# Kernel tuning notes

Hardware: AMD Instinct MI355X
Metric: run time of the kernel (lower is better)

The kernel has to match this reference:

```python
import jax, jax.numpy as jnp
import numpy as np

EPS = 0.97  # ContrastLoss eps
T = 0.07    # temperature

def _embed(x, W, b):
    # Linear + L2 normalize (Normalize(power=2))
    h = x @ W.T + b                     # [B, feat_dim]
    norm = jnp.sqrt(jnp.sum(h * h, axis=1, keepdims=True))
    return h / norm

def setup_inputs() -> dict:
    key = jax.random.key(0)
    ks = jax.random.split(key, 7)
    B, S, Td, F = 8192, 2048, 2048, 128
    return {
        "f_s": jax.random.normal(ks[0], (B, S), jnp.float32),
        "f_t": jax.random.normal(ks[1], (B, Td), jnp.float32),
        "y": jax.random.randint(ks[2], (B,), 0, 100, jnp.int64),
        "W_s": jax.random.normal(ks[3], (F, S), jnp.float32) * 0.02,
        "b_s": jax.random.normal(ks[4], (F,), jnp.float32) * 0.02,
        "W_t": jax.random.normal(ks[5], (F, Td), jnp.float32) * 0.02,
        "b_t": jax.random.normal(ks[6], (F,), jnp.float32) * 0.02,
    }

def reference(f_s, f_t, y, W_s, b_s, W_t, b_t):
    fs = _embed(f_s, W_s, b_s)
    ft = _embed(f_t, W_t, b_t)
    # CRDLoss re-normalizes (idempotent, kept for fidelity)
    fs = fs / jnp.linalg.norm(fs, axis=1, keepdims=True)
    ft = ft / jnp.linalg.norm(ft, axis=1, keepdims=True)
    bsz = fs.shape[0]
    x = jnp.exp((fs @ ft.T) / T)  # [B, B] exponentiated similarities
    same = y[None, :] == y[:, None]        # y_expand == y_expand.T
    diag = jnp.eye(bsz, dtype=bool)
    pos_mask = same & ~diag
    neg_mask = ~same & ~diag
    # masked log-ratio sums instead of dynamic-shape gathers
    log_D1 = jnp.log(x / (x + EPS))
    log_D0 = jnp.log(EPS / (x + EPS))
    loss = -(jnp.sum(jnp.where(pos_mask, log_D1, 0.0))
             + jnp.sum(jnp.where(neg_mask, log_D0, 0.0))) / bsz
    return loss
```

## Files before the change

kernel.cpp:

```cpp
#include <hip/hip_runtime.h>
#include <math.h>


typedef _Float16 half_t;
typedef half_t halfx4 __attribute__((ext_vector_type(4)));
typedef half_t halfx8 __attribute__((ext_vector_type(8)));
typedef float f32x4 __attribute__((ext_vector_type(4)));

#define B_TOT   8192
#define K_EMB   2048
#define F_DIM   128
#define INV_T   14.285714285714286f
#define EPS_C   0.97f
#define LOG_EPS (-0.030459207485f)

__global__ __launch_bounds__(256) void cvt_w_kernel(
    const float* __restrict__ Ws, const float* __restrict__ Wt,
    half_t* __restrict__ Ws16, half_t* __restrict__ Wt16)
{
    const float* src = blockIdx.y ? Wt : Ws;
    half_t* dst = blockIdx.y ? Wt16 : Ws16;
    int pos4 = blockIdx.x * 256 + threadIdx.x;
    float4 v = *(const float4*)(src + (size_t)pos4 * 4);
    halfx4 h4 = {(half_t)v.x, (half_t)v.y, (half_t)v.z, (half_t)v.w};
    *(halfx4*)(dst + (size_t)pos4 * 4) = h4;
}

__global__ __launch_bounds__(256) void embed_kernel(
    const float* __restrict__ Xs, const float* __restrict__ Xt,
    const half_t* __restrict__ Ws16, const half_t* __restrict__ Wt16,
    const float* __restrict__ bs, const float* __restrict__ bt,
    half_t* __restrict__ outs, half_t* __restrict__ outt)
{
    const float* X; const half_t* W16; const float* bias; half_t* out;
    if (blockIdx.y == 0) { X = Xs; W16 = Ws16; bias = bs; out = outs; }
    else                 { X = Xt; W16 = Wt16; bias = bt; out = outt; }

    __shared__ half_t As[2][32][72];
    __shared__ half_t Bs[2][128][72];
    __shared__ float  biasS[128];
    __shared__ float  redS[32][2];
    __shared__ float  invS[32];

    const int tid = threadIdx.x;
    const int r0  = blockIdx.x * 32;
    if (tid < 128) biasS[tid] = bias[tid];

    const int lane = tid & 63;
    const int w    = tid >> 6;
    const int wm   = w & 1, wn = w >> 1;
    const int l16  = lane & 15, lhi = lane >> 4;

    f32x4 acc[4];
    for (int in = 0; in < 4; ++in) acc[in] = f32x4{0.f, 0.f, 0.f, 0.f};

    const int ar0 = tid >> 4, ar1 = (tid + 256) >> 4;
    const int akq = (tid & 15) * 4;
    const int bc  = (tid & 7) * 8;

    float4 na[2]; uint4 nb[4];

    na[0] = *(const float4*)(X + (size_t)(r0 + ar0) * K_EMB + akq);
    na[1] = *(const float4*)(X + (size_t)(r0 + ar1) * K_EMB + akq);
#pragma unroll
    for (int i = 0; i < 4; ++i)
        nb[i] = *(const uint4*)(W16 + (size_t)((tid + i * 256) >> 3) * K_EMB + bc);
    {
        halfx4 h0 = {(half_t)na[0].x, (half_t)na[0].y, (half_t)na[0].z, (half_t)na[0].w};
        halfx4 h1 = {(half_t)na[1].x, (half_t)na[1].y, (half_t)na[1].z, (half_t)na[1].w};
        *(halfx4*)&As[0][ar0][akq] = h0;
        *(halfx4*)&As[0][ar1][akq] = h1;
#pragma unroll
        for (int i = 0; i < 4; ++i)
            *(uint4*)&Bs[0][(tid + i * 256) >> 3][bc] = nb[i];
    }
    __syncthreads();

    for (int it = 0; it < 32; ++it) {
        const int cur = it & 1;
        if (it < 31) {
            const int kb = (it + 1) * 64;
            na[0] = *(const float4*)(X + (size_t)(r0 + ar0) * K_EMB + kb + akq);
            na[1] = *(const float4*)(X + (size_t)(r0 + ar1) * K_EMB + kb + akq);
#pragma unroll
            for (int i = 0; i < 4; ++i)
                nb[i] = *(const uint4*)(W16 + (size_t)((tid + i * 256) >> 3) * K_EMB + kb + bc);
        }
#pragma unroll
        for (int kk = 0; kk < 2; ++kk) {
            halfx8 a, b[4];
            a = *(const halfx8*)&As[cur][wm * 16 + l16][kk * 32 + lhi * 8];
#pragma unroll
            for (int in = 0; in < 4; ++in)
                b[in] = *(const halfx8*)&Bs[cur][wn * 64 + in * 16 + l16][kk * 32 + lhi * 8];
#pragma unroll
            for (int in = 0; in < 4; ++in)
                acc[in] = __builtin_amdgcn_mfma_f32_16x16x32_f16(a, b[in], acc[in], 0, 0, 0);
        }
        if (it < 31) {
            const int nxt = cur ^ 1;
            halfx4 h0 = {(half_t)na[0].x, (half_t)na[0].y, (half_t)na[0].z, (half_t)na[0].w};
            halfx4 h1 = {(half_t)na[1].x, (half_t)na[1].y, (half_t)na[1].z, (half_t)na[1].w};
            *(halfx4*)&As[nxt][ar0][akq] = h0;
            *(halfx4*)&As[nxt][ar1][akq] = h1;
#pragma unroll
            for (int i = 0; i < 4; ++i)
                *(uint4*)&Bs[nxt][(tid + i * 256) >> 3][bc] = nb[i];
        }
        __syncthreads();
    }

    float h[4][4];
    float psum[4];
#pragma unroll
    for (int reg = 0; reg < 4; ++reg) {
        float p = 0.f;
#pragma unroll
        for (int in = 0; in < 4; ++in) {
            int col = wn * 64 + in * 16 + l16;
            float v = acc[in][reg] + biasS[col];
            h[in][reg] = v;
            p += v * v;
        }
        p += __shfl_xor(p, 1);
        p += __shfl_xor(p, 2);
        p += __shfl_xor(p, 4);
        p += __shfl_xor(p, 8);
        psum[reg] = p;
    }
    if (l16 == 0)
#pragma unroll
        for (int reg = 0; reg < 4; ++reg)
            redS[wm * 16 + lhi * 4 + reg][wn] = psum[reg];
    __syncthreads();
    if (tid < 32) invS[tid] = rsqrtf(redS[tid][0] + redS[tid][1]);
    __syncthreads();

#pragma unroll
    for (int in = 0; in < 4; ++in)
#pragma unroll
        for (int reg = 0; reg < 4; ++reg) {
            int row = wm * 16 + lhi * 4 + reg;
            int col = wn * 64 + in * 16 + l16;
            out[(size_t)(r0 + row) * F_DIM + col] = (half_t)(h[in][reg] * invS[row]);
        }
}

__global__ __launch_bounds__(256) void loss_kernel(
    const half_t* __restrict__ FS, const half_t* __restrict__ FT,
    const int* __restrict__ y, double* __restrict__ partials)
{
    __shared__ uint4 As4[128 * 8];
    __shared__ uint4 Bs4[128 * 8];
    __shared__ int   yrl[128], ycl[128];
    __shared__ float wsum[4];

    const int tid = threadIdx.x;
    const int i0  = blockIdx.x * 128;
    const int j0  = blockIdx.y * 128;

    if (tid < 128) yrl[tid] = y[i0 + tid];
    else           ycl[tid - 128] = y[j0 + tid - 128];

    const int lane = tid & 63;
    const int w    = tid >> 6;
    const int wm   = w >> 1, wn = w & 1;
    const int l16  = lane & 15, lhi = lane >> 4;

#pragma unroll
    for (int i = 0; i < 4; ++i) {
        int f = tid + i * 256;
        int row = f >> 3, c = f & 7;
        As4[row * 8 + (c ^ (row & 7))] = *(const uint4*)(FS + (size_t)(i0 + row) * F_DIM + c * 8);
    }
#pragma unroll
    for (int i = 0; i < 4; ++i) {
        int f = tid + i * 256;
        int row = f >> 3, c = f & 7;
        Bs4[row * 8 + (c ^ (row & 7))] = *(const uint4*)(FT + (size_t)(j0 + row) * F_DIM + c * 8);
    }
    __syncthreads();

    f32x4 acc[4][4];
    for (int im = 0; im < 4; ++im)
        for (int in = 0; in < 4; ++in)
            acc[im][in] = f32x4{0.f, 0.f, 0.f, 0.f};

    for (int kc = 0; kc < 2; ++kc) {
#pragma unroll
        for (int kk = 0; kk < 2; ++kk) {
            halfx8 a[4], b[4];
#pragma unroll
            for (int im = 0; im < 4; ++im) {
                int r = wm * 64 + im * 16 + l16;
                a[im] = *(const halfx8*)&As4[r * 8 + ((kk * 4 + lhi) ^ (r & 7))];
            }
#pragma unroll
            for (int in = 0; in < 4; ++in) {
                int r = wn * 64 + in * 16 + l16;
                b[in] = *(const halfx8*)&Bs4[r * 8 + ((kk * 4 + lhi) ^ (r & 7))];
            }
#pragma unroll
            for (int im = 0; im < 4; ++im)
#pragma unroll
                for (int in = 0; in < 4; ++in)
                    acc[im][in] = __builtin_amdgcn_mfma_f32_16x16x32_f16(
                        a[im], b[in], acc[im][in], 0, 0, 0);
        }
        if (kc == 0) {
            __syncthreads();
#pragma unroll
            for (int i = 0; i < 4; ++i) {
                int f = tid + i * 256;
                int row = f >> 3, c = f & 7;
                As4[row * 8 + (c ^ (row & 7))] =
                    *(const uint4*)(FS + (size_t)(i0 + row) * F_DIM + 64 + c * 8);
            }
#pragma unroll
            for (int i = 0; i < 4; ++i) {
                int f = tid + i * 256;
                int row = f >> 3, c = f & 7;
                Bs4[row * 8 + (c ^ (row & 7))] =
                    *(const uint4*)(FT + (size_t)(j0 + row) * F_DIM + 64 + c * 8);
            }
            __syncthreads();
        }
    }

    float local = 0.f;
    for (int im = 0; im < 4; ++im) {
        for (int reg = 0; reg < 4; ++reg) {
            int il = wm * 64 + im * 16 + lhi * 4 + reg;
            int yi = yrl[il];
            int gi = i0 + il;
            for (int in = 0; in < 4; ++in) {
                int jl = wn * 64 + in * 16 + l16;
                float s  = acc[im][in][reg];
                float sT = s * INV_T;
                float e  = __expf(sT);
                float l  = __logf(e + EPS_C);
                float term = (yi == ycl[jl]) ? (sT - l) : (LOG_EPS - l);
                if (gi != (j0 + jl)) local += term;
            }
        }
    }
    for (int m = 1; m < 64; m <<= 1) local += __shfl_xor(local, m);
    if (lane == 0) wsum[w] = local;
    __syncthreads();
    if (tid == 0)
        partials[blockIdx.y * gridDim.x + blockIdx.x] =
            ((double)wsum[0] + (double)wsum[1]) + ((double)wsum[2] + (double)wsum[3]);
}

__global__ __launch_bounds__(256) void finalize_kernel(
    const double* __restrict__ partials, float* __restrict__ out)
{
    __shared__ double sh[4];
    double loc = 0.0;
    for (int i = threadIdx.x; i < 4096; i += 256) loc += partials[i];
    for (int m = 1; m < 64; m <<= 1) loc += __shfl_xor(loc, m);
    int lane = threadIdx.x & 63, w = threadIdx.x >> 6;
    if (lane == 0) sh[w] = loc;
    __syncthreads();
    if (threadIdx.x == 0)
        out[0] = (float)(-(sh[0] + sh[1] + sh[2] + sh[3]) / (double)B_TOT);
}

extern "C" void kernel_launch(void* const* d_in, const int* in_sizes, int n_in,
                              void* d_out, int out_size, void* d_ws, size_t ws_size,
                              hipStream_t stream)
{
    const size_t WS_NEEDED = (64 << 10) + (4 << 20) + (1 << 20);
    if (ws_size < WS_NEEDED) return;

    const float* f_s = (const float*)d_in[0];
    const float* f_t = (const float*)d_in[1];
    const int*   y   = (const int*)d_in[2];
    const float* W_s = (const float*)d_in[3];
    const float* b_s = (const float*)d_in[4];
    const float* W_t = (const float*)d_in[5];
    const float* b_t = (const float*)d_in[6];
    float* out = (float*)d_out;

    char* ws = (char*)d_ws;
    double* partials = (double*)ws;
    half_t* fs   = (half_t*)(ws + (64 << 10));
    half_t* ft   = (half_t*)(ws + (64 << 10) + (2 << 20));
    half_t* Ws16 = (half_t*)(ws + (64 << 10) + (4 << 20));
    half_t* Wt16 = (half_t*)(ws + (64 << 10) + (4 << 20) + (512 << 10));

    cvt_w_kernel<<<dim3(256, 2), 256, 0, stream>>>(W_s, W_t, Ws16, Wt16);
    embed_kernel<<<dim3(256, 2), 256, 0, stream>>>(f_s, f_t, Ws16, Wt16, b_s, b_t, fs, ft);
    loss_kernel<<<dim3(64, 64), 256, 0, stream>>>(fs, ft, y, partials);
    finalize_kernel<<<1, 256, 0, stream>>>(partials, out);
    (void)in_sizes; (void)n_in; (void)out_size;
}
```

Before: 213.5 us.

## Restructure embed GEMM with deeper register prefetch, XOR-swizzled LDS and BK=128

Rewrites the embedding GEMM main loop. The K tile grows from 64 to 128, two register sets keep two global loads in flight (double-buffered prefetch), and shared-memory padding is replaced by an XOR swizzle. It also adds a lighter barrier (lgkmcnt wait plus s_barrier), moves the bias into registers, and sets launch_bounds(256,2). The aim is to hide global-load latency on this memory-bound fp32 input read and to cut LDS bank conflicts, at the cost of more register pressure.

```diff
diff --git a/kernel.cpp b/kernel.cpp
--- a/kernel.cpp
+++ b/kernel.cpp
@@ -26,7 +26,14 @@
     *(halfx4*)(dst + (size_t)pos4 * 4) = h4;
 }
 
-__global__ __launch_bounds__(256) void embed_kernel(
+__device__ __forceinline__ void cvst(uint4* dst, float4 x, float4 y)
+{
+    halfx8 h = {(half_t)x.x, (half_t)x.y, (half_t)x.z, (half_t)x.w,
+                (half_t)y.x, (half_t)y.y, (half_t)y.z, (half_t)y.w};
+    *(halfx8*)dst = h;
+}
+
+__global__ __launch_bounds__(256, 2) void embed_kernel(
     const float* __restrict__ Xs, const float* __restrict__ Xt,
     const half_t* __restrict__ Ws16, const half_t* __restrict__ Wt16,
     const float* __restrict__ bs, const float* __restrict__ bt,
@@ -36,90 +43,111 @@
     if (blockIdx.y == 0) { X = Xs; W16 = Ws16; bias = bs; out = outs; }
     else                 { X = Xt; W16 = Wt16; bias = bt; out = outt; }
 
-    __shared__ half_t As[2][32][72];
-    __shared__ half_t Bs[2][128][72];
-    __shared__ float  biasS[128];
-    __shared__ float  redS[32][2];
-    __shared__ float  invS[32];
-
-    const int tid = threadIdx.x;
-    const int r0  = blockIdx.x * 32;
-    if (tid < 128) biasS[tid] = bias[tid];
-
+    __shared__ uint4 smem[5120];
+
+    const int tid  = threadIdx.x;
+    const int r0   = blockIdx.x * 32;
     const int lane = tid & 63;
     const int w    = tid >> 6;
     const int wm   = w & 1, wn = w >> 1;
     const int l16  = lane & 15, lhi = lane >> 4;
 
+    float bv[4];
+#pragma unroll
+    for (int in = 0; in < 4; ++in) bv[in] = bias[wn * 64 + in * 16 + l16];
+
+    const int ar0 = tid >> 4;
+    const int ac  = tid & 15;
+    const int axr = ac ^ ar0;
+    const int adst0 = ar0 * 16 + axr;
+    const int adst1 = adst0 + 256;
+    const float* aptr0 = X + (size_t)(r0 + ar0) * K_EMB + ac * 8;
+    const float* aptr1 = aptr0 + (size_t)16 * K_EMB;
+    const half_t* bptr = W16 + (size_t)ar0 * K_EMB + ac * 8;
+
     f32x4 acc[4];
+#pragma unroll
     for (int in = 0; in < 4; ++in) acc[in] = f32x4{0.f, 0.f, 0.f, 0.f};
 
-    const int ar0 = tid >> 4, ar1 = (tid + 256) >> 4;
-    const int akq = (tid & 15) * 4;
-    const int bc  = (tid & 7) * 8;
-
-    float4 na[2]; uint4 nb[4];
-
-    na[0] = *(const float4*)(X + (size_t)(r0 + ar0) * K_EMB + akq);
-    na[1] = *(const float4*)(X + (size_t)(r0 + ar1) * K_EMB + akq);
-#pragma unroll
-    for (int i = 0; i < 4; ++i)
-        nb[i] = *(const uint4*)(W16 + (size_t)((tid + i * 256) >> 3) * K_EMB + bc);
-    {
-        halfx4 h0 = {(half_t)na[0].x, (half_t)na[0].y, (half_t)na[0].z, (half_t)na[0].w};
-        halfx4 h1 = {(half_t)na[1].x, (half_t)na[1].y, (half_t)na[1].z, (half_t)na[1].w};
-        *(halfx4*)&As[0][ar0][akq] = h0;
-        *(halfx4*)&As[0][ar1][akq] = h1;
-#pragma unroll
-        for (int i = 0; i < 4; ++i)
-            *(uint4*)&Bs[0][(tid + i * 256) >> 3][bc] = nb[i];
-    }
-    __syncthreads();
-
-    for (int it = 0; it < 32; ++it) {
-        const int cur = it & 1;
-        if (it < 31) {
-            const int kb = (it + 1) * 64;
-            na[0] = *(const float4*)(X + (size_t)(r0 + ar0) * K_EMB + kb + akq);
-            na[1] = *(const float4*)(X + (size_t)(r0 + ar1) * K_EMB + kb + akq);
-#pragma unroll
-            for (int i = 0; i < 4; ++i)
-                nb[i] = *(const uint4*)(W16 + (size_t)((tid + i * 256) >> 3) * K_EMB + kb + bc);
-        }
-#pragma unroll
-        for (int kk = 0; kk < 2; ++kk) {
-            halfx8 a, b[4];
-            a = *(const halfx8*)&As[cur][wm * 16 + l16][kk * 32 + lhi * 8];
-#pragma unroll
-            for (int in = 0; in < 4; ++in)
-                b[in] = *(const halfx8*)&Bs[cur][wn * 64 + in * 16 + l16][kk * 32 + lhi * 8];
-#pragma unroll
-            for (int in = 0; in < 4; ++in)
-                acc[in] = __builtin_amdgcn_mfma_f32_16x16x32_f16(a, b[in], acc[in], 0, 0, 0);
-        }
-        if (it < 31) {
-            const int nxt = cur ^ 1;
-            halfx4 h0 = {(half_t)na[0].x, (half_t)na[0].y, (half_t)na[0].z, (half_t)na[0].w};
-            halfx4 h1 = {(half_t)na[1].x, (half_t)na[1].y, (half_t)na[1].z, (half_t)na[1].w};
-            *(halfx4*)&As[nxt][ar0][akq] = h0;
-            *(halfx4*)&As[nxt][ar1][akq] = h1;
-#pragma unroll
-            for (int i = 0; i < 4; ++i)
-                *(uint4*)&Bs[nxt][(tid + i * 256) >> 3][bc] = nb[i];
-        }
-        __syncthreads();
-    }
-
-    float h[4][4];
+    float4 aR0[4], aR1[4];
+    uint4  bR0[8], bR1[8];
+
+#define LOADT(aR, bR, KB) do {                                                 \
+        aR[0] = *(const float4*)(aptr0 + (KB));                                \
+        aR[1] = *(const float4*)(aptr0 + (KB) + 4);                            \
+        aR[2] = *(const float4*)(aptr1 + (KB));                                \
+        aR[3] = *(const float4*)(aptr1 + (KB) + 4);                            \
+        _Pragma("unroll")                                                      \
+        for (int i = 0; i < 8; ++i)                                            \
+            bR[i] = *(const uint4*)(bptr + (KB) + (size_t)i * 16 * K_EMB);     \
+    } while (0)
+
+#define STORET(aR, bR, BUF) do {                                               \
+        cvst(&smem[(BUF) * 512 + adst0], aR[0], aR[1]);                        \
+        cvst(&smem[(BUF) * 512 + adst1], aR[2], aR[3]);                        \
+        _Pragma("unroll")                                                      \
+        for (int i = 0; i < 8; ++i)                                            \
+            smem[1024 + (BUF) * 2048 + adst0 + i * 256] = bR[i];               \
+    } while (0)
+
+#define COMPUTE(BUF) do {                                                      \
+        _Pragma("unroll")                                                      \
+        for (int kk = 0; kk < 4; ++kk) {                                       \
+            const int sl = (kk * 4 + lhi) ^ l16;                               \
+            halfx8 afrag = *(const halfx8*)&smem[(BUF) * 512 +                 \
+                                                 (wm * 16 + l16) * 16 + sl];   \
+            _Pragma("unroll")                                                  \
+            for (int in = 0; in < 4; ++in) {                                   \
+                halfx8 bfrag = *(const halfx8*)&smem[1024 + (BUF) * 2048 +     \
+                                     (wn * 64 + in * 16 + l16) * 16 + sl];     \
+                acc[in] = __builtin_amdgcn_mfma_f32_16x16x32_f16(              \
+                    afrag, bfrag, acc[in], 0, 0, 0);                           \
+            }                                                                  \
+        }                                                                      \
+    } while (0)
+
+#define BARRIER() do {                                                         \
+        asm volatile("s_waitcnt lgkmcnt(0)" ::: "memory");                     \
+        __builtin_amdgcn_s_barrier();                                          \
+    } while (0)
+
+    LOADT(aR0, bR0, 0);
+    STORET(aR0, bR0, 0);
+    LOADT(aR1, bR1, 128);
+    BARRIER();
+
+    for (int itp = 0; itp < 14; itp += 2) {
+        LOADT(aR0, bR0, (itp + 2) * 128);
+        COMPUTE(0);
+        STORET(aR1, bR1, 1);
+        BARRIER();
+        LOADT(aR1, bR1, (itp + 3) * 128);
+        COMPUTE(1);
+        STORET(aR0, bR0, 0);
+        BARRIER();
+    }
+    COMPUTE(0);
+    STORET(aR1, bR1, 1);
+    BARRIER();
+    COMPUTE(1);
+
+#undef LOADT
+#undef STORET
+#undef COMPUTE
+#undef BARRIER
+
+    float* redS = (float*)smem;
+    float* invS = ((float*)smem) + 64;
+
+    float hh[4][4];
     float psum[4];
 #pragma unroll
     for (int reg = 0; reg < 4; ++reg) {
         float p = 0.f;
 #pragma unroll
         for (int in = 0; in < 4; ++in) {
-            int col = wn * 64 + in * 16 + l16;
-            float v = acc[in][reg] + biasS[col];
-            h[in][reg] = v;
+            float v = acc[in][reg] + bv[in];
+            hh[in][reg] = v;
             p += v * v;
         }
         p += __shfl_xor(p, 1);
@@ -131,9 +159,9 @@
     if (l16 == 0)
 #pragma unroll
         for (int reg = 0; reg < 4; ++reg)
-            redS[wm * 16 + lhi * 4 + reg][wn] = psum[reg];
-    __syncthreads();
-    if (tid < 32) invS[tid] = rsqrtf(redS[tid][0] + redS[tid][1]);
+            redS[(wm * 16 + lhi * 4 + reg) * 2 + wn] = psum[reg];
+    __syncthreads();
+    if (tid < 32) invS[tid] = rsqrtf(redS[tid * 2] + redS[tid * 2 + 1]);
     __syncthreads();
 
 #pragma unroll
@@ -142,7 +170,7 @@
         for (int reg = 0; reg < 4; ++reg) {
             int row = wm * 16 + lhi * 4 + reg;
             int col = wn * 64 + in * 16 + l16;
-            out[(size_t)(r0 + row) * F_DIM + col] = (half_t)(h[in][reg] * invS[row]);
+            out[(size_t)(r0 + row) * F_DIM + col] = (half_t)(hh[in][reg] * invS[row]);
         }
 }
 
```

Result: slower. 285.1 us (+33.6%).
